# Performance work log

Hardware: AMD Instinct MI355X
Metric: run time of the kernel (lower is better)

Reference implementation:

```python
import jax, jax.numpy as jnp
import numpy as np

N = 100000


def gcn_conv(x, edge_index, W, b):
    """PyG GCNConv: add self-loops, symmetric normalization, x @ W, aggregate, + bias."""
    n = x.shape[0]
    src = jnp.concatenate([edge_index[0], jnp.arange(n)])
    dst = jnp.concatenate([edge_index[1], jnp.arange(n)])
    deg = jax.ops.segment_sum(jnp.ones_like(dst, dtype=x.dtype), dst, num_segments=n)
    dinv = jnp.where(deg > 0, jax.lax.rsqrt(deg), 0.0)
    norm = dinv[src] * dinv[dst]  # [E+N]
    h = x @ W  # [N, out]
    msg = h[src] * norm[:, None]  # gather + scale
    agg = jax.ops.segment_sum(msg, dst, num_segments=n)
    return agg + b


def setup_inputs() -> dict:
    key = jax.random.key(0)
    ks = jax.random.split(key, 10)
    x = jax.random.normal(ks[0], (N, 256), dtype=jnp.float32)
    edge_index = jax.random.randint(ks[1], (2, 3200000), 0, N, dtype=jnp.int64)
    def glorot(k, fan_in, fan_out):
        s = np.sqrt(6.0 / (fan_in + fan_out)).astype(np.float32)
        return jax.random.uniform(k, (fan_in, fan_out), jnp.float32, -s, s)
    return {
        "x": x,
        "edge_index": edge_index,
        "W1": glorot(ks[2], 256, 128), "b1": jnp.zeros((128,), jnp.float32),
        "W2": glorot(ks[3], 128, 64), "b2": jnp.zeros((64,), jnp.float32),
        "W3": glorot(ks[4], 64, 16), "b3": jnp.zeros((16,), jnp.float32),
        "Wc": glorot(ks[5], 16, 2), "bc": jnp.zeros((2,), jnp.float32),
    }


def reference(x, edge_index, W1, b1, W2, b2, W3, b3, Wc, bc):
    h = jnp.tanh(gcn_conv(x, edge_index, W1, b1))
    h = jnp.tanh(gcn_conv(h, edge_index, W2, b2))
    h = jnp.tanh(gcn_conv(h, edge_index, W3, b3))
    out = h @ Wc + bc
    return (out, h)
```

## Files before the change

kernel.cpp:

```cpp
#include <hip/hip_runtime.h>
#include <hip/hip_fp16.h>
#include <cstdint>
#include <cstddef>


#define EPB 16384
#define BSHIFT 8
#define NBUC_MAX 512
#define BCAP 12800

__global__ __launch_bounds__(256) void scan_block(const int* __restrict__ src, int n,
                                                  int* __restrict__ incl,
                                                  int* __restrict__ bsum) {
    int tid = threadIdx.x;
    int v = blockIdx.x * 256 + tid;
    int val = (v < n) ? src[v] : 0;
    int lane = tid & 63, w = tid >> 6;
#pragma unroll
    for (int off = 1; off < 64; off <<= 1) {
        int t = __shfl_up(val, off, 64);
        if (lane >= off) val += t;
    }
    __shared__ int wsum[4];
    if (lane == 63) wsum[w] = val;
    __syncthreads();
#pragma unroll
    for (int i = 0; i < 4; ++i)
        if (i < w) val += wsum[i];
    if (v < n) incl[v] = val;
    if (tid == 255) bsum[blockIdx.x] = val;
}

__global__ __launch_bounds__(512) void scan_sums(int* __restrict__ bsum, int nb) {
    int tid = threadIdx.x;
    int val = (tid < nb) ? bsum[tid] : 0;
    int lane = tid & 63, w = tid >> 6;
#pragma unroll
    for (int off = 1; off < 64; off <<= 1) {
        int t = __shfl_up(val, off, 64);
        if (lane >= off) val += t;
    }
    __shared__ int wsum[8];
    if (lane == 63) wsum[w] = val;
    __syncthreads();
#pragma unroll
    for (int i = 0; i < 8; ++i)
        if (i < w) val += wsum[i];
    if (tid < nb) bsum[tid] = val;
}

__global__ __launch_bounds__(256) void finalize_scan(
    const int* __restrict__ incl, const int* __restrict__ bsum,
    const int* __restrict__ src, int n, int* __restrict__ excl) {
    int v = blockIdx.x * 256 + threadIdx.x;
    if (v >= n) return;
    int boff = (blockIdx.x == 0) ? 0 : bsum[blockIdx.x - 1];
    excl[v] = boff + incl[v] - src[v];
}

__global__ __launch_bounds__(256) void hist_bucket(
    const int* __restrict__ ei, int E, int nbuc, int nch,
    int* __restrict__ histG) {
    __shared__ int h[NBUC_MAX];
    const int k = blockIdx.x;
    for (int b = threadIdx.x; b < NBUC_MAX; b += 256) h[b] = 0;
    __syncthreads();
    const int base = k * EPB, end = min(E, base + EPB);
    for (int i = base + threadIdx.x; i < end; i += 256)
        atomicAdd(&h[ei[(size_t)E + i] >> BSHIFT], 1);
    __syncthreads();
    for (int b = threadIdx.x; b < nbuc; b += 256)
        histG[(size_t)b * nch + k] = h[b];
}

__global__ __launch_bounds__(256) void bucket_scatter(
    const int* __restrict__ ei, int E, int nbuc, int nch,
    const int* __restrict__ offs, uint2* __restrict__ ebuf) {
    __shared__ int cur[NBUC_MAX];
    const int k = blockIdx.x;
    for (int b = threadIdx.x; b < nbuc; b += 256)
        cur[b] = offs[(size_t)b * nch + k];
    __syncthreads();
    const int base = k * EPB, end = min(E, base + EPB);
    for (int i = base + threadIdx.x; i < end; i += 256) {
        int s = ei[i];
        int d = ei[(size_t)E + i];
        int pos = atomicAdd(&cur[d >> BSHIFT], 1);
        ebuf[pos] = make_uint2((unsigned)s, (unsigned)d);
    }
}

__global__ __launch_bounds__(256) void bucket_build(
    const uint2* __restrict__ ebuf, const int* __restrict__ offs,
    int E, int nbuc, int nch, int n,
    int* __restrict__ col, int* __restrict__ deg,
    int* __restrict__ row_start, float* __restrict__ dinv) {
    const int b = blockIdx.x;
    const int tid = threadIdx.x;
    const int estart = offs[(size_t)b * nch];
    const int eend = (b + 1 < nbuc) ? offs[(size_t)(b + 1) * nch] : E;
    const int cnt = eend - estart;

    __shared__ int degl[256];
    __shared__ int curl[256];
    __shared__ int wsum[4];
    __shared__ int colstage[BCAP];

    degl[tid] = 0;
    __syncthreads();
    for (int i = tid; i < cnt; i += 256)
        atomicAdd(&degl[ebuf[estart + i].y & 255], 1);
    __syncthreads();
    int myDeg = degl[tid];
    int val = myDeg;
    int lane = tid & 63, w = tid >> 6;
#pragma unroll
    for (int off = 1; off < 64; off <<= 1) {
        int t = __shfl_up(val, off, 64);
        if (lane >= off) val += t;
    }
    if (lane == 63) wsum[w] = val;
    __syncthreads();
#pragma unroll
    for (int i = 0; i < 4; ++i)
        if (i < w) val += wsum[i];
    int excl = val - myDeg;
    curl[tid] = excl;
    int v = (b << BSHIFT) + tid;
    if (v < n) {
        deg[v] = myDeg;
        row_start[v] = estart + excl;
        dinv[v] = rsqrtf((float)(myDeg + 1));
    }
    __syncthreads();
    if (cnt <= BCAP) {
        for (int i = tid; i < cnt; i += 256) {
            uint2 e = ebuf[estart + i];
            int pos = atomicAdd(&curl[e.y & 255], 1);
            colstage[pos] = (int)e.x;
        }
        __syncthreads();
        for (int i = tid; i < cnt; i += 256)
            col[estart + i] = colstage[i];
    } else {
        for (int i = tid; i < cnt; i += 256) {
            uint2 e = ebuf[estart + i];
            int pos = atomicAdd(&curl[e.y & 255], 1);
            col[estart + pos] = (int)e.x;
        }
    }
}

__device__ inline unsigned int pack2h(float a, float b) {
    __half ha = __float2half_rn(a), hb = __float2half_rn(b);
    unsigned short ua = *(unsigned short*)&ha, ub = *(unsigned short*)&hb;
    return (unsigned int)ua | ((unsigned int)ub << 16);
}

template <int FIN, int FOUT, int TM>
__global__ __launch_bounds__(256) void gemm_tile_h(
    const float* __restrict__ X, const float* __restrict__ W,
    const float* __restrict__ dinv, __half* __restrict__ Hs, int n) {
    constexpr int CT = FOUT / 4;
    constexpr int RG = 256 / CT;
    static_assert(TM == RG * 4, "tile mismatch");
    constexpr int LROW = FIN + 4;
    __shared__ float xs[TM][LROW];

    const int node0 = blockIdx.x * TM;
    const int tid = threadIdx.x;

    constexpr int C4 = FIN / 4;
    for (int i = tid; i < TM * C4; i += 256) {
        int r = i / C4, c = i % C4;
        float4 v = make_float4(0.f, 0.f, 0.f, 0.f);
        if (node0 + r < n) v = *(const float4*)(X + (size_t)(node0 + r) * FIN + c * 4);
        *(float4*)&xs[r][c * 4] = v;
    }
    __syncthreads();

    const int col = (tid % CT) * 4;
    const int r0 = (tid / CT) * 4;

    float acc[4][4];
#pragma unroll
    for (int i = 0; i < 4; ++i)
#pragma unroll
        for (int j = 0; j < 4; ++j) acc[i][j] = 0.f;

#pragma unroll 8
    for (int k = 0; k < FIN; ++k) {
        float4 b = *(const float4*)(W + (size_t)k * FOUT + col);
        float a0 = xs[r0 + 0][k];
        float a1 = xs[r0 + 1][k];
        float a2 = xs[r0 + 2][k];
        float a3 = xs[r0 + 3][k];
        acc[0][0] = fmaf(a0, b.x, acc[0][0]); acc[0][1] = fmaf(a0, b.y, acc[0][1]);
        acc[0][2] = fmaf(a0, b.z, acc[0][2]); acc[0][3] = fmaf(a0, b.w, acc[0][3]);
        acc[1][0] = fmaf(a1, b.x, acc[1][0]); acc[1][1] = fmaf(a1, b.y, acc[1][1]);
        acc[1][2] = fmaf(a1, b.z, acc[1][2]); acc[1][3] = fmaf(a1, b.w, acc[1][3]);
        acc[2][0] = fmaf(a2, b.x, acc[2][0]); acc[2][1] = fmaf(a2, b.y, acc[2][1]);
        acc[2][2] = fmaf(a2, b.z, acc[2][2]); acc[2][3] = fmaf(a2, b.w, acc[2][3]);
        acc[3][0] = fmaf(a3, b.x, acc[3][0]); acc[3][1] = fmaf(a3, b.y, acc[3][1]);
        acc[3][2] = fmaf(a3, b.z, acc[3][2]); acc[3][3] = fmaf(a3, b.w, acc[3][3]);
    }

#pragma unroll
    for (int rr = 0; rr < 4; ++rr) {
        int node = node0 + r0 + rr;
        if (node < n) {
            float di = dinv[node];
            uint2 pk;
            pk.x = pack2h(acc[rr][0] * di, acc[rr][1] * di);
            pk.y = pack2h(acc[rr][2] * di, acc[rr][3] * di);
            *(uint2*)(Hs + (size_t)node * FOUT + col) = pk;
        }
    }
}

__device__ inline void add8h(float* acc, uint4 p) {
    unsigned int w[4] = {p.x, p.y, p.z, p.w};
#pragma unroll
    for (int t = 0; t < 4; ++t) {
        __half2 h = *(const __half2*)&w[t];
        float2 f = __half22float2(h);
        acc[2 * t] += f.x;
        acc[2 * t + 1] += f.y;
    }
}

template <int F>
__global__ __launch_bounds__(256) void pull_agg_h(
    const int* __restrict__ row_start, const int* __restrict__ deg,
    const int* __restrict__ col, const __half* __restrict__ Hs,
    const float* __restrict__ dinv, const float* __restrict__ B,
    float* __restrict__ OUT, int n) {
    constexpr int TPE = F / 8;
    long long gid = (long long)blockIdx.x * 256 + threadIdx.x;
    int node = (int)(gid / TPE);
    int lane = (int)(gid % TPE);
    if (node >= n) return;
    const int beg = row_start[node];
    const int cnt = deg[node];
    const size_t lo = (size_t)lane * 8;

    float acc[8] = {0.f, 0.f, 0.f, 0.f, 0.f, 0.f, 0.f, 0.f};
    add8h(acc, *(const uint4*)(Hs + (size_t)node * F + lo));

    int j = 0;
    for (; j + 4 <= cnt; j += 4) {
        int s0 = col[beg + j + 0], s1 = col[beg + j + 1];
        int s2 = col[beg + j + 2], s3 = col[beg + j + 3];
        uint4 p0 = *(const uint4*)(Hs + (size_t)s0 * F + lo);
        uint4 p1 = *(const uint4*)(Hs + (size_t)s1 * F + lo);
        uint4 p2 = *(const uint4*)(Hs + (size_t)s2 * F + lo);
        uint4 p3 = *(const uint4*)(Hs + (size_t)s3 * F + lo);
        add8h(acc, p0); add8h(acc, p1); add8h(acc, p2); add8h(acc, p3);
    }
    for (; j < cnt; ++j) {
        int s = col[beg + j];
        add8h(acc, *(const uint4*)(Hs + (size_t)s * F + lo));
    }

    float di = dinv[node];
    float4 b0 = *(const float4*)(B + lo);
    float4 b1 = *(const float4*)(B + lo + 4);
    float4 r0, r1;
    r0.x = tanhf(fmaf(acc[0], di, b0.x));
    r0.y = tanhf(fmaf(acc[1], di, b0.y));
    r0.z = tanhf(fmaf(acc[2], di, b0.z));
    r0.w = tanhf(fmaf(acc[3], di, b0.w));
    r1.x = tanhf(fmaf(acc[4], di, b1.x));
    r1.y = tanhf(fmaf(acc[5], di, b1.y));
    r1.z = tanhf(fmaf(acc[6], di, b1.z));
    r1.w = tanhf(fmaf(acc[7], di, b1.w));
    float* op = OUT + (size_t)node * F + lo;
    *(float4*)(op) = r0;
    *(float4*)(op + 4) = r1;
}

__global__ void classifier_kernel(const float* __restrict__ Hf,
                                  const float* __restrict__ Wc,
                                  const float* __restrict__ bc,
                                  float* __restrict__ out, int n) {
    int v = blockIdx.x * blockDim.x + threadIdx.x;
    if (v >= n) return;
    float o0 = bc[0], o1 = bc[1];
    const float* h = Hf + (size_t)v * 16;
#pragma unroll
    for (int k = 0; k < 16; ++k) {
        float hv = h[k];
        o0 = fmaf(hv, Wc[k * 2 + 0], o0);
        o1 = fmaf(hv, Wc[k * 2 + 1], o1);
    }
    out[(size_t)v * 2 + 0] = o0;
    out[(size_t)v * 2 + 1] = o1;
}

extern "C" void kernel_launch(void* const* d_in, const int* in_sizes, int n_in,
                              void* d_out, int out_size, void* d_ws, size_t ws_size,
                              hipStream_t stream) {
    const float* x  = (const float*)d_in[0];
    const int* ei   = (const int*)d_in[1];
    const float* W1 = (const float*)d_in[2];
    const float* b1 = (const float*)d_in[3];
    const float* W2 = (const float*)d_in[4];
    const float* b2 = (const float*)d_in[5];
    const float* W3 = (const float*)d_in[6];
    const float* b3 = (const float*)d_in[7];
    const float* Wc = (const float*)d_in[8];
    const float* bc = (const float*)d_in[9];

    const int n = in_sizes[0] / 256;
    const int E = in_sizes[1] / 2;
    const int nbuc = (n + 255) >> BSHIFT;
    const int nch  = (E + EPB - 1) / EPB;
    const int NH   = nbuc * nch;
    const int nb2  = (NH + 255) / 256;

    float* outp = (float*)d_out;
    float* outh = outp + (size_t)n * 2;

    int*    deg       = (int*)d_ws;
    float*  dinv      = (float*)d_ws + (size_t)n;
    int*    row_start = (int*)d_ws + 2 * (size_t)n;
    int*    histG     = (int*)d_ws + 3 * (size_t)n;
    int*    incl      = histG + NH;
    int*    bsum      = incl + NH;
    int*    offs      = bsum + 512;
    int*    col       = offs + NH;
    __half* HsH       = (__half*)(col + E);
    float*  xbuf      = (float*)(HsH + (size_t)n * 128);
    uint2*  ebuf      = (uint2*)xbuf;

    hist_bucket<<<nch, 256, 0, stream>>>(ei, E, nbuc, nch, histG);
    scan_block<<<nb2, 256, 0, stream>>>(histG, NH, incl, bsum);
    scan_sums<<<1, 512, 0, stream>>>(bsum, nb2);
    finalize_scan<<<nb2, 256, 0, stream>>>(incl, bsum, histG, NH, offs);
    bucket_scatter<<<nch, 256, 0, stream>>>(ei, E, nbuc, nch, offs, ebuf);
    bucket_build<<<nbuc, 256, 0, stream>>>(ebuf, offs, E, nbuc, nch, n,
                                           col, deg, row_start, dinv);

    gemm_tile_h<256, 128, 32><<<(n + 31) / 32, 256, 0, stream>>>(x, W1, dinv, HsH, n);
    pull_agg_h<128><<<(int)(((long long)n * 16 + 255) / 256), 256, 0, stream>>>(
        row_start, deg, col, HsH, dinv, b1, xbuf, n);

    gemm_tile_h<128, 64, 64><<<(n + 63) / 64, 256, 0, stream>>>(xbuf, W2, dinv, HsH, n);
    pull_agg_h<64><<<(int)(((long long)n * 8 + 255) / 256), 256, 0, stream>>>(
        row_start, deg, col, HsH, dinv, b2, xbuf, n);

    gemm_tile_h<64, 16, 256><<<(n + 255) / 256, 256, 0, stream>>>(xbuf, W3, dinv, HsH, n);
    pull_agg_h<16><<<(int)(((long long)n * 2 + 255) / 256), 256, 0, stream>>>(
        row_start, deg, col, HsH, dinv, b3, outh, n);

    classifier_kernel<<<(n + 255) / 256, 256, 0, stream>>>(outh, Wc, bc, outp, n);
}
```

Measured before the change: 725.9 us.

## Split half-precision feature matrix into 32-column planes for cache-resident aggregation

The GEMM now writes its fp16 output in column planes 32 features wide (16 for the last layer) instead of full-width rows. Aggregation then runs one pull kernel per plane, so each pass gathers from a 6.4 MB plane that may stay resident in L2/LLC rather than the whole feature matrix. The cost is re-reading the CSR column indices and row metadata once per plane, extra kernel launches, and narrower 64-byte gathers per edge.

```diff
diff --git a/kernel.cpp b/kernel.cpp
--- a/kernel.cpp
+++ b/kernel.cpp
@@ -157,8 +157,8 @@
     return (unsigned int)ua | ((unsigned int)ub << 16);
 }
 
-template <int FIN, int FOUT, int TM>
-__global__ __launch_bounds__(256) void gemm_tile_h(
+template <int FIN, int FOUT, int TM, int PLANEW>
+__global__ __launch_bounds__(256) void gemm_tile_p(
     const float* __restrict__ X, const float* __restrict__ W,
     const float* __restrict__ dinv, __half* __restrict__ Hs, int n) {
     constexpr int CT = FOUT / 4;
@@ -205,6 +205,9 @@
         acc[3][2] = fmaf(a3, b.z, acc[3][2]); acc[3][3] = fmaf(a3, b.w, acc[3][3]);
     }
 
+    const int plane = col / PLANEW;
+    const int c = col % PLANEW;
+    __half* base = Hs + (size_t)plane * ((size_t)n * PLANEW) + c;
 #pragma unroll
     for (int rr = 0; rr < 4; ++rr) {
         int node = node0 + r0 + rr;
@@ -213,7 +216,7 @@
             uint2 pk;
             pk.x = pack2h(acc[rr][0] * di, acc[rr][1] * di);
             pk.y = pack2h(acc[rr][2] * di, acc[rr][3] * di);
-            *(uint2*)(Hs + (size_t)node * FOUT + col) = pk;
+            *(uint2*)(base + (size_t)node * PLANEW) = pk;
         }
     }
 }
@@ -229,13 +232,13 @@
     }
 }
 
-template <int F>
-__global__ __launch_bounds__(256) void pull_agg_h(
+template <int PLANEW, int OUTSTRIDE>
+__global__ __launch_bounds__(256) void pull_plane(
     const int* __restrict__ row_start, const int* __restrict__ deg,
-    const int* __restrict__ col, const __half* __restrict__ Hs,
-    const float* __restrict__ dinv, const float* __restrict__ B,
-    float* __restrict__ OUT, int n) {
-    constexpr int TPE = F / 8;
+    const int* __restrict__ col, const __half* __restrict__ HsP,
+    const float* __restrict__ dinv, const float* __restrict__ Bp,
+    float* __restrict__ OUTp, int n) {
+    constexpr int TPE = PLANEW / 8;
     long long gid = (long long)blockIdx.x * 256 + threadIdx.x;
     int node = (int)(gid / TPE);
     int lane = (int)(gid % TPE);
@@ -245,26 +248,26 @@
     const size_t lo = (size_t)lane * 8;
 
     float acc[8] = {0.f, 0.f, 0.f, 0.f, 0.f, 0.f, 0.f, 0.f};
-    add8h(acc, *(const uint4*)(Hs + (size_t)node * F + lo));
+    add8h(acc, *(const uint4*)(HsP + (size_t)node * PLANEW + lo));
 
     int j = 0;
     for (; j + 4 <= cnt; j += 4) {
         int s0 = col[beg + j + 0], s1 = col[beg + j + 1];
         int s2 = col[beg + j + 2], s3 = col[beg + j + 3];
-        uint4 p0 = *(const uint4*)(Hs + (size_t)s0 * F + lo);
-        uint4 p1 = *(const uint4*)(Hs + (size_t)s1 * F + lo);
-        uint4 p2 = *(const uint4*)(Hs + (size_t)s2 * F + lo);
-        uint4 p3 = *(const uint4*)(Hs + (size_t)s3 * F + lo);
+        uint4 p0 = *(const uint4*)(HsP + (size_t)s0 * PLANEW + lo);
+        uint4 p1 = *(const uint4*)(HsP + (size_t)s1 * PLANEW + lo);
+        uint4 p2 = *(const uint4*)(HsP + (size_t)s2 * PLANEW + lo);
+        uint4 p3 = *(const uint4*)(HsP + (size_t)s3 * PLANEW + lo);
         add8h(acc, p0); add8h(acc, p1); add8h(acc, p2); add8h(acc, p3);
     }
     for (; j < cnt; ++j) {
         int s = col[beg + j];
-        add8h(acc, *(const uint4*)(Hs + (size_t)s * F + lo));
+        add8h(acc, *(const uint4*)(HsP + (size_t)s * PLANEW + lo));
     }
 
     float di = dinv[node];
-    float4 b0 = *(const float4*)(B + lo);
-    float4 b1 = *(const float4*)(B + lo + 4);
+    float4 b0 = *(const float4*)(Bp + lo);
+    float4 b1 = *(const float4*)(Bp + lo + 4);
     float4 r0, r1;
     r0.x = tanhf(fmaf(acc[0], di, b0.x));
     r0.y = tanhf(fmaf(acc[1], di, b0.y));
@@ -274,7 +277,7 @@
     r1.y = tanhf(fmaf(acc[5], di, b1.y));
     r1.z = tanhf(fmaf(acc[6], di, b1.z));
     r1.w = tanhf(fmaf(acc[7], di, b1.w));
-    float* op = OUT + (size_t)node * F + lo;
+    float* op = OUTp + (size_t)node * OUTSTRIDE + lo;
     *(float4*)(op) = r0;
     *(float4*)(op + 4) = r1;
 }
@@ -333,6 +336,8 @@
     float*  xbuf      = (float*)(HsH + (size_t)n * 128);
     uint2*  ebuf      = (uint2*)xbuf;
 
+    const size_t PS = (size_t)n * 32;
+
     hist_bucket<<<nch, 256, 0, stream>>>(ei, E, nbuc, nch, histG);
     scan_block<<<nb2, 256, 0, stream>>>(histG, NH, incl, bsum);
     scan_sums<<<1, 512, 0, stream>>>(bsum, nb2);
@@ -341,16 +346,22 @@
     bucket_build<<<nbuc, 256, 0, stream>>>(ebuf, offs, E, nbuc, nch, n,
                                            col, deg, row_start, dinv);
 
-    gemm_tile_h<256, 128, 32><<<(n + 31) / 32, 256, 0, stream>>>(x, W1, dinv, HsH, n);
-    pull_agg_h<128><<<(int)(((long long)n * 16 + 255) / 256), 256, 0, stream>>>(
-        row_start, deg, col, HsH, dinv, b1, xbuf, n);
-
-    gemm_tile_h<128, 64, 64><<<(n + 63) / 64, 256, 0, stream>>>(xbuf, W2, dinv, HsH, n);
-    pull_agg_h<64><<<(int)(((long long)n * 8 + 255) / 256), 256, 0, stream>>>(
-        row_start, deg, col, HsH, dinv, b2, xbuf, n);
-
-    gemm_tile_h<64, 16, 256><<<(n + 255) / 256, 256, 0, stream>>>(xbuf, W3, dinv, HsH, n);
-    pull_agg_h<16><<<(int)(((long long)n * 2 + 255) / 256), 256, 0, stream>>>(
+    const int pblk32 = (int)(((long long)n * 4 + 255) / 256);
+
+    gemm_tile_p<256, 128, 32, 32><<<(n + 31) / 32, 256, 0, stream>>>(x, W1, dinv, HsH, n);
+    for (int p = 0; p < 4; ++p)
+        pull_plane<32, 128><<<pblk32, 256, 0, stream>>>(
+            row_start, deg, col, HsH + (size_t)p * PS, dinv, b1 + p * 32,
+            xbuf + p * 32, n);
+
+    gemm_tile_p<128, 64, 64, 32><<<(n + 63) / 64, 256, 0, stream>>>(xbuf, W2, dinv, HsH, n);
+    for (int p = 0; p < 2; ++p)
+        pull_plane<32, 64><<<pblk32, 256, 0, stream>>>(
+            row_start, deg, col, HsH + (size_t)p * PS, dinv, b2 + p * 32,
+            xbuf + p * 32, n);
+
+    gemm_tile_p<64, 16, 256, 16><<<(n + 255) / 256, 256, 0, stream>>>(xbuf, W3, dinv, HsH, n);
+    pull_plane<16, 16><<<(int)(((long long)n * 2 + 255) / 256), 256, 0, stream>>>(
         row_start, deg, col, HsH, dinv, b3, outh, n);
 
     classifier_kernel<<<(n + 255) / 256, 256, 0, stream>>>(outh, Wc, bc, outp, n);
```

Result: slower. 842.7 us (+16.1%).
